# Performance work log

Measured on AMD Instinct MI355X. Metric: run time of the kernel, lower is better.

## Reference

```python
import jax, jax.numpy as jnp
import numpy as np

B, C, L = 32, 128, 4096          # batch, n_channels, signal length
P, Q = 100, 20                   # n_projections, n_quantiles


def setup_inputs() -> dict:
    key = jax.random.key(0)
    k1, k2, k3, k4 = jax.random.split(key, 4)
    X = jax.random.normal(k1, (B, C, L), dtype=jnp.float32)
    # conv1d kernel of shape (P, C, 1) collapsed to (P, C)
    W = jax.random.normal(k2, (P, C), dtype=jnp.float32)
    s = 2.33 * jnp.sqrt(jnp.float32(C))
    min_vals = -s + 0.1 * jax.random.normal(k3, (P,), dtype=jnp.float32)
    max_vals = s + 0.1 * jax.random.normal(k4, (P,), dtype=jnp.float32)
    return {"X": X, "W": W, "min_vals": min_vals, "max_vals": max_vals}


def reference(X, W, min_vals, max_vals):
    # kernel-size-1 conv1d == channel projection
    a = jnp.einsum('bcl,pc->bpl', X, W)  # [B, P, L]
    fracs = jnp.arange(1, Q + 1, dtype=a.dtype) / jnp.asarray(Q + 1, a.dtype)
    thr = min_vals[None, :] + (max_vals - min_vals)[None, :] * fracs[:, None]  # [Q, P]

    def body(carry, t):  # t: [P] thresholds for one quantile
        cdf_q = jnp.mean((a < t[None, :, None]).astype(a.dtype), axis=-1)  # [B, P]
        return carry, cdf_q

    _, cdf = jax.lax.scan(body, None, thr)          # [Q, B, P]
    cdf = jnp.transpose(cdf, (1, 2, 0))             # [B, P, Q]
    return cdf.reshape(B, P * Q)
```

## Files before the change

kernel.cpp:

```cpp
#include <hip/hip_runtime.h>
#include <hip/hip_bf16.h>

#define B_   32
#define C_   128
#define L_   4096
#define P_   100
#define NPT  7
#define Q_   20
#define NBIN 21
#define NCH  (NPT * 4)
#define HSZ  (P_ * NBIN)

typedef short          bf16x8 __attribute__((ext_vector_type(8)));
typedef float          f32x4  __attribute__((ext_vector_type(4)));
typedef unsigned short u16x8  __attribute__((ext_vector_type(8)));

__device__ float mn_c[P_];
__device__ float invd_c[P_];

__device__ inline unsigned short f2bf(float f) {
    __hip_bfloat16 h = __float2bfloat16(f);
    unsigned short u; __builtin_memcpy(&u, &h, 2);
    return u;
}

__global__ void prep_kernel(const float* __restrict__ W, const float* __restrict__ minv,
                            const float* __restrict__ maxv, unsigned short* __restrict__ Wf) {
    const int t = blockIdx.x * 256 + threadIdx.x;
    if (t < NCH * 64) {
        const int chunk = t >> 6, lane = t & 63;
        const int pt = chunk >> 2, ks = chunk & 3;
        const int p  = pt * 16 + (lane & 15);
        const int c0 = ks * 32 + (lane >> 4) * 8;
        u16x8 v;
#pragma unroll
        for (int j = 0; j < 8; ++j)
            v[j] = (p < P_) ? f2bf(W[p * C_ + c0 + j]) : (unsigned short)0;
        *(u16x8*)(Wf + (size_t)t * 8) = v;
    } else if (t >= NCH * 64 && t < NCH * 64 + P_) {
        const int p = t - NCH * 64;
        const float mn = minv[p];
        mn_c[p]   = mn;
        invd_c[p] = (float)NBIN / (maxv[p] - mn);
    }
}

__global__ __launch_bounds__(256, 2)
void radon_dma_kernel(const float* __restrict__ X, const unsigned short* __restrict__ Wf,
                      float* __restrict__ out) {
    __shared__ float Xlds[C_ * 128];
    __shared__ int   hist[HSZ];

    const int tid  = threadIdx.x;
    const int b    = blockIdx.y;
    const int lblk = blockIdx.x;
    const int wave = tid >> 6;
    const int lane = tid & 63;
    const int quad = lane >> 4;
    const int nn   = lane & 15;

    {
        const float* gb = X + ((size_t)b * C_ + (lane >> 5)) * L_ + lblk * 128 + (lane & 31) * 4;
#pragma unroll
        for (int i = 0; i < 16; ++i) {
            const int c0 = wave * 32 + i * 2;
            __builtin_amdgcn_global_load_lds(
                (const __attribute__((address_space(1))) unsigned int*)(gb + (size_t)c0 * L_),
                (__attribute__((address_space(3))) unsigned int*)&Xlds[c0 * 128],
                16, 0, 0);
        }
    }
    for (int i = tid; i < HSZ; i += 256) hist[i] = 0;
    __syncthreads();

    bf16x8 bfrag[2][4];
#pragma unroll
    for (int lt = 0; lt < 2; ++lt) {
        const int ll = wave * 32 + lt * 16 + nn;
#pragma unroll
        for (int ks = 0; ks < 4; ++ks) {
            float xf[8];
#pragma unroll
            for (int j = 0; j < 8; ++j)
                xf[j] = Xlds[(ks * 32 + quad * 8 + j) * 128 + ll];
            unsigned int u[4];
#pragma unroll
            for (int jp = 0; jp < 4; ++jp) {
                __hip_bfloat162 h2 = __float22bfloat162_rn(
                    make_float2(xf[2 * jp], xf[2 * jp + 1]));
                __builtin_memcpy(&u[jp], &h2, 4);
            }
            __builtin_memcpy(&bfrag[lt][ks], u, 16);
        }
    }

    for (int pt = 0; pt < NPT; ++pt) {
        bf16x8 afrag[4];
#pragma unroll
        for (int ks = 0; ks < 4; ++ks)
            afrag[ks] = *(const bf16x8*)(Wf + ((size_t)(pt * 4 + ks) * 64 + lane) * 8);

        f32x4 acc0 = {0.f, 0.f, 0.f, 0.f};
        f32x4 acc1 = {0.f, 0.f, 0.f, 0.f};
#pragma unroll
        for (int ks = 0; ks < 4; ++ks) {
            acc0 = __builtin_amdgcn_mfma_f32_16x16x32_bf16(afrag[ks], bfrag[0][ks], acc0, 0, 0, 0);
            acc1 = __builtin_amdgcn_mfma_f32_16x16x32_bf16(afrag[ks], bfrag[1][ks], acc1, 0, 0, 0);
        }

#pragma unroll
        for (int r = 0; r < 4; ++r) {
            const int p = pt * 16 + quad * 4 + r;
            if (p < P_) {
                const float mn   = mn_c[p];
                const float invd = invd_c[p];
                {
                    const float t = (acc0[r] - mn) * invd;
                    int k = 0;
                    if (t > 0.f) { const int ki = (int)t; k = (ki > 20) ? 20 : ki; }
                    atomicAdd(&hist[p * NBIN + k], 1);
                }
                {
                    const float t = (acc1[r] - mn) * invd;
                    int k = 0;
                    if (t > 0.f) { const int ki = (int)t; k = (ki > 20) ? 20 : ki; }
                    atomicAdd(&hist[p * NBIN + k], 1);
                }
            }
        }
    }
    __syncthreads();

    for (int i = tid; i < P_ * Q_; i += 256) {
        const int p  = i / Q_;
        const int qi = i - p * Q_;
        int s = 0;
        for (int k = 0; k <= qi; ++k) s += hist[p * NBIN + k];
        atomicAdd(&out[((size_t)b * P_ + p) * Q_ + qi], (float)s * (1.0f / (float)L_));
    }
}

extern "C" void kernel_launch(void* const* d_in, const int* in_sizes, int n_in,
                              void* d_out, int out_size, void* d_ws, size_t ws_size,
                              hipStream_t stream) {
    const float* X  = (const float*)d_in[0];
    const float* W  = (const float*)d_in[1];
    const float* mn = (const float*)d_in[2];
    const float* mx = (const float*)d_in[3];
    float* out = (float*)d_out;
    unsigned short* Wf = (unsigned short*)d_ws;

    hipMemsetAsync(out, 0, (size_t)out_size * sizeof(float), stream);
    prep_kernel<<<8, 256, 0, stream>>>(W, mn, mx, Wf);

    dim3 grid(L_ / 128, B_);
    radon_dma_kernel<<<grid, dim3(256), 0, stream>>>(X, Wf, out);
}
```

Before: 119.3 us.

## Double-buffer channel chunks in LDS and widen L tile to 256

Each block now covers 256 signal positions with 512 threads, instead of 128 positions with 256 threads. X is streamed through two 32-channel LDS buffers, so the async load of the next K-chunk overlaps the bf16 conversion and MFMAs of the current chunk. Accumulators for all projection tiles stay in registers until the histogram stage. This halves the number of blocks and the per-block histogram flush atomics to global memory. The costs are higher register pressure from keeping 14 accumulators live and a barrier per chunk that likely also waits on the in-flight prefetch.

```diff
diff --git a/kernel.cpp b/kernel.cpp
--- a/kernel.cpp
+++ b/kernel.cpp
@@ -10,6 +10,8 @@
 #define NBIN 21
 #define NCH  (NPT * 4)
 #define HSZ  (P_ * NBIN)
+#define LT_  256
+#define TPB  512
 
 typedef short          bf16x8 __attribute__((ext_vector_type(8)));
 typedef float          f32x4  __attribute__((ext_vector_type(4)));
@@ -45,11 +47,12 @@
     }
 }
 
-__global__ __launch_bounds__(256, 2)
-void radon_dma_kernel(const float* __restrict__ X, const unsigned short* __restrict__ Wf,
-                      float* __restrict__ out) {
-    __shared__ float Xlds[C_ * 128];
-    __shared__ int   hist[HSZ];
+__global__ __launch_bounds__(TPB, 4)
+void radon_pipe_kernel(const float* __restrict__ X, const unsigned short* __restrict__ Wf,
+                       float* __restrict__ out) {
+    __shared__ __align__(16) float Xb0[32 * LT_];
+    __shared__ __align__(16) float Xb1[32 * LT_];
+    __shared__ int hist[HSZ];
 
     const int tid  = threadIdx.x;
     const int b    = blockIdx.y;
@@ -59,30 +62,46 @@
     const int quad = lane >> 4;
     const int nn   = lane & 15;
 
-    {
-        const float* gb = X + ((size_t)b * C_ + (lane >> 5)) * L_ + lblk * 128 + (lane & 31) * 4;
+    const float* gsrc = X + (size_t)b * C_ * L_ + lblk * LT_ + lane * 4;
+
+#define ISSUE_Q(KS, DST) do {                                                        \
+    const float* s_ = gsrc + (size_t)((KS) * 32 + wave * 4) * L_;                    \
+    float* d_ = (DST) + (wave * 4) * LT_;                                            \
+    _Pragma("unroll")                                                                \
+    for (int i_ = 0; i_ < 4; ++i_)                                                   \
+        __builtin_amdgcn_global_load_lds(                                            \
+            (const __attribute__((address_space(1))) unsigned int*)(s_ + (size_t)i_ * L_), \
+            (__attribute__((address_space(3))) unsigned int*)(d_ + i_ * LT_),        \
+            16, 0, 0);                                                               \
+} while (0)
+
+    f32x4 acc[NPT][2];
 #pragma unroll
-        for (int i = 0; i < 16; ++i) {
-            const int c0 = wave * 32 + i * 2;
-            __builtin_amdgcn_global_load_lds(
-                (const __attribute__((address_space(1))) unsigned int*)(gb + (size_t)c0 * L_),
-                (__attribute__((address_space(3))) unsigned int*)&Xlds[c0 * 128],
-                16, 0, 0);
-        }
+    for (int pt = 0; pt < NPT; ++pt) {
+        acc[pt][0] = (f32x4){0.f, 0.f, 0.f, 0.f};
+        acc[pt][1] = (f32x4){0.f, 0.f, 0.f, 0.f};
     }
-    for (int i = tid; i < HSZ; i += 256) hist[i] = 0;
+
+    ISSUE_Q(0, Xb0);
+    for (int i = tid; i < HSZ; i += TPB) hist[i] = 0;
     __syncthreads();
 
-    bf16x8 bfrag[2][4];
 #pragma unroll
-    for (int lt = 0; lt < 2; ++lt) {
-        const int ll = wave * 32 + lt * 16 + nn;
+    for (int ks = 0; ks < 4; ++ks) {
+        const float* curb = (ks & 1) ? Xb1 : Xb0;
+        if (ks < 3) {
+            if ((ks + 1) & 1) ISSUE_Q(ks + 1, Xb1);
+            else              ISSUE_Q(ks + 1, Xb0);
+        }
+
+        bf16x8 bfrag[2];
 #pragma unroll
-        for (int ks = 0; ks < 4; ++ks) {
+        for (int lt = 0; lt < 2; ++lt) {
+            const int ll = wave * 32 + lt * 16 + nn;
             float xf[8];
 #pragma unroll
             for (int j = 0; j < 8; ++j)
-                xf[j] = Xlds[(ks * 32 + quad * 8 + j) * 128 + ll];
+                xf[j] = curb[(quad * 8 + j) * LT_ + ll];
             unsigned int u[4];
 #pragma unroll
             for (int jp = 0; jp < 4; ++jp) {
@@ -90,54 +109,44 @@
                     make_float2(xf[2 * jp], xf[2 * jp + 1]));
                 __builtin_memcpy(&u[jp], &h2, 4);
             }
-            __builtin_memcpy(&bfrag[lt][ks], u, 16);
+            __builtin_memcpy(&bfrag[lt], u, 16);
         }
+
+#pragma unroll
+        for (int pt = 0; pt < NPT; ++pt) {
+            const bf16x8 af = *(const bf16x8*)(Wf + ((size_t)(pt * 4 + ks) * 64 + lane) * 8);
+            acc[pt][0] = __builtin_amdgcn_mfma_f32_16x16x32_bf16(af, bfrag[0], acc[pt][0], 0, 0, 0);
+            acc[pt][1] = __builtin_amdgcn_mfma_f32_16x16x32_bf16(af, bfrag[1], acc[pt][1], 0, 0, 0);
+        }
+        __syncthreads();
     }
 
-    for (int pt = 0; pt < NPT; ++pt) {
-        bf16x8 afrag[4];
 #pragma unroll
-        for (int ks = 0; ks < 4; ++ks)
-            afrag[ks] = *(const bf16x8*)(Wf + ((size_t)(pt * 4 + ks) * 64 + lane) * 8);
-
-        f32x4 acc0 = {0.f, 0.f, 0.f, 0.f};
-        f32x4 acc1 = {0.f, 0.f, 0.f, 0.f};
-#pragma unroll
-        for (int ks = 0; ks < 4; ++ks) {
-            acc0 = __builtin_amdgcn_mfma_f32_16x16x32_bf16(afrag[ks], bfrag[0][ks], acc0, 0, 0, 0);
-            acc1 = __builtin_amdgcn_mfma_f32_16x16x32_bf16(afrag[ks], bfrag[1][ks], acc1, 0, 0, 0);
-        }
-
+    for (int pt = 0; pt < NPT; ++pt)
 #pragma unroll
         for (int r = 0; r < 4; ++r) {
             const int p = pt * 16 + quad * 4 + r;
             if (p < P_) {
-                const float mn   = mn_c[p];
-                const float invd = invd_c[p];
-                {
-                    const float t = (acc0[r] - mn) * invd;
-                    int k = 0;
-                    if (t > 0.f) { const int ki = (int)t; k = (ki > 20) ? 20 : ki; }
-                    atomicAdd(&hist[p * NBIN + k], 1);
-                }
-                {
-                    const float t = (acc1[r] - mn) * invd;
+                const float mn = mn_c[p], invd = invd_c[p];
+#pragma unroll
+                for (int lt = 0; lt < 2; ++lt) {
+                    const float t = (acc[pt][lt][r] - mn) * invd;
                     int k = 0;
                     if (t > 0.f) { const int ki = (int)t; k = (ki > 20) ? 20 : ki; }
                     atomicAdd(&hist[p * NBIN + k], 1);
                 }
             }
         }
-    }
     __syncthreads();
 
-    for (int i = tid; i < P_ * Q_; i += 256) {
+    for (int i = tid; i < P_ * Q_; i += TPB) {
         const int p  = i / Q_;
         const int qi = i - p * Q_;
         int s = 0;
         for (int k = 0; k <= qi; ++k) s += hist[p * NBIN + k];
         atomicAdd(&out[((size_t)b * P_ + p) * Q_ + qi], (float)s * (1.0f / (float)L_));
     }
+#undef ISSUE_Q
 }
 
 extern "C" void kernel_launch(void* const* d_in, const int* in_sizes, int n_in,
@@ -153,6 +162,6 @@
     hipMemsetAsync(out, 0, (size_t)out_size * sizeof(float), stream);
     prep_kernel<<<8, 256, 0, stream>>>(W, mn, mx, Wf);
 
-    dim3 grid(L_ / 128, B_);
-    radon_dma_kernel<<<grid, dim3(256), 0, stream>>>(X, Wf, out);
+    dim3 grid(L_ / LT_, B_);
+    radon_pipe_kernel<<<grid, dim3(TPB), 0, stream>>>(X, Wf, out);
 }
```

Result: no change. 117.7 us (-1.4%).
